# Kernel tuning notes

Measured on AMD Instinct MI355X. Metric: run time of the kernel, lower is better.

The kernel has to match this reference:

```python
import jax, jax.numpy as jnp
import numpy as np

B, H, W, D = 8, 32, 32, 512
NH = 8
DK = DV = 512
DKH = DK // NH
DVH = DV // NH


def setup_inputs() -> dict:
    key = jax.random.key(0)
    ks = jax.random.split(key, 16)
    s = 0.02
    return {
        "q": jax.random.normal(ks[0], (B, H, W, D), dtype=jnp.float32),
        "k": jax.random.normal(ks[1], (B, H, W, D), dtype=jnp.float32),
        "q_mask": jax.random.randint(ks[2], (B, H, W), 0, 2).astype(bool),
        "k_mask": jax.random.randint(ks[3], (B, H, W), 0, 2).astype(bool),
        "pos_logits": jax.random.normal(ks[4], (B, H, W, H, W), dtype=jnp.float32),
        "Wq": jax.random.normal(ks[5], (D, DK), dtype=jnp.float32) * s,
        "bq": jnp.zeros((DK,), dtype=jnp.float32),
        "Wk": jax.random.normal(ks[6], (D, DK), dtype=jnp.float32) * s,
        "bk": jnp.zeros((DK,), dtype=jnp.float32),
        "Wv": jax.random.normal(ks[7], (DK, DV), dtype=jnp.float32) * s,
        "bv": jnp.zeros((DV,), dtype=jnp.float32),
        "Wo": jax.random.normal(ks[8], (DV, D), dtype=jnp.float32) * s,
        "bo": jnp.zeros((D,), dtype=jnp.float32),
    }


def _split_heads(x, nh):
    b, h, w, d = x.shape
    return x.reshape(b, h, w, nh, d // nh).transpose(0, 3, 1, 2, 4)  # [B,Nh,H,W,dh]


def reference(q, k, q_mask, k_mask, pos_logits, Wq, bq, Wk, bk, Wv, bv, Wo, bo):
    b, h, w, d = q.shape
    qp = (q @ Wq + bq) * (DKH ** -0.5)
    kp = k @ Wk + bk
    vp = kp @ Wv + bv  # faithful quirk: v = projv(projk(k))
    qs = _split_heads(qp, NH)  # [B,Nh,H,W,dkh]
    ks_ = _split_heads(kp, NH)
    vs = _split_heads(vp, NH)  # [B,Nh,H,W,dvh]
    # additive mask: -inf where exactly one of q_mask[i,j], k_mask[k,l] is set
    xor = q_mask[:, :, :, None, None] ^ k_mask[:, None, None, :, :]  # [B,H,W,H,W]
    attn_mask = jnp.where(xor, -jnp.inf, 0.0)[:, None]  # [B,1,H,W,H,W]
    con = jnp.einsum('bhijd,bhkld->bhijkl', qs, ks_)  # [B,Nh,H,W,H,W]
    logits = attn_mask + con + pos_logits[:, None]
    weights = jax.nn.softmax(logits.reshape(b, NH, h, w, h * w), axis=-1)
    weights = weights.reshape(b, NH, h, w, h, w)
    attn = jnp.einsum('bhijkl,bhkld->bhijd', weights, vs)  # [B,Nh,H,W,dvh]
    attn = attn.transpose(0, 2, 3, 1, 4).reshape(b, h, w, NH * DVH)
    return attn @ Wo + bo  # dropout is identity at inference
```

## Files before the change

kernel.cpp:

```cpp
#include <hip/hip_runtime.h>
#include <hip/hip_bf16.h>
#include <math.h>

#define TOK 8192
#define DMODEL 512
#define SEQ 1024
#define NHEADS 8
#define DH 64
#define NBATCH 8

typedef __attribute__((ext_vector_type(8))) short short8v;
typedef __attribute__((ext_vector_type(4))) float f32x4;
typedef __attribute__((ext_vector_type(4))) int i32x4;

#define MFMA16(a, b, c) __builtin_amdgcn_mfma_f32_16x16x32_bf16(a, b, c, 0, 0, 0)

__device__ __forceinline__ unsigned short f2bf(float x) {
  __hip_bfloat16 h = __float2bfloat16(x);
  unsigned short u;
  __builtin_memcpy(&u, &h, 2);
  return u;
}
__device__ __forceinline__ unsigned int pk2(float a, float b) {
  return (unsigned int)f2bf(a) | ((unsigned int)f2bf(b) << 16);
}

__global__ __launch_bounds__(256) void wtr4_kernel(
    const float* __restrict__ W0, const float* __restrict__ W1,
    const float* __restrict__ W2, const float* __restrict__ W3,
    unsigned short* __restrict__ T0, unsigned short* __restrict__ T1,
    unsigned short* __restrict__ T2, unsigned short* __restrict__ T3) {
  __shared__ unsigned short tile[64][72];
  const int z = blockIdx.z;
  const float* W = (z == 0) ? W0 : (z == 1) ? W1 : (z == 2) ? W2 : W3;
  unsigned short* Wt = (z == 0) ? T0 : (z == 1) ? T1 : (z == 2) ? T2 : T3;
  const int kt = blockIdx.x, nt = blockIdx.y;
  const int t = threadIdx.x, r = t >> 2, c0 = (t & 3) * 16;
  const float* src = W + (size_t)(kt * 64 + r) * 512 + nt * 64 + c0;
  short8v v0, v1;
#pragma unroll
  for (int e = 0; e < 4; ++e) {
    float4 f = *reinterpret_cast<const float4*>(src + e * 4);
    short* dstv = (e < 2) ? (short*)&v0 : (short*)&v1;
    dstv[(e & 1) * 4 + 0] = (short)f2bf(f.x);
    dstv[(e & 1) * 4 + 1] = (short)f2bf(f.y);
    dstv[(e & 1) * 4 + 2] = (short)f2bf(f.z);
    dstv[(e & 1) * 4 + 3] = (short)f2bf(f.w);
  }
  *reinterpret_cast<short8v*>(&tile[r][c0]) = v0;
  *reinterpret_cast<short8v*>(&tile[r][c0 + 8]) = v1;
  __syncthreads();
  short8v o0, o1;
#pragma unroll
  for (int e = 0; e < 8; ++e) o0[e] = (short)tile[c0 + e][r];
#pragma unroll
  for (int e = 0; e < 8; ++e) o1[e] = (short)tile[c0 + 8 + e][r];
  unsigned short* dst = Wt + (size_t)(nt * 64 + r) * 512 + kt * 64 + c0;
  *reinterpret_cast<short8v*>(dst) = o0;
  *reinterpret_cast<short8v*>(dst + 8) = o1;
}

template <int AF32, int OUTMODE>
__device__ __forceinline__ void gemm_body(
    const void* __restrict__ Ap, const unsigned short* __restrict__ Wt,
    const float* __restrict__ bias, float scale, void* __restrict__ Cout) {
  __shared__ unsigned short Asl[128][72];
  __shared__ unsigned short Bsl[128][72];
  const int t = threadIdx.x;
  const int w = t >> 6, lane = t & 63, li = lane & 15, lg = lane >> 4;
  const int wr = w >> 1, wc = w & 1;
  const int rowBase = blockIdx.y * 128, colBase = blockIdx.x * 128;

  f32x4 zero4 = {0.f, 0.f, 0.f, 0.f};
  f32x4 acc[4][4];
#pragma unroll
  for (int mi = 0; mi < 4; ++mi)
#pragma unroll
    for (int nj = 0; nj < 4; ++nj) acc[mi][nj] = zero4;

  const int sr = t >> 1, sh = (t & 1) * 32;

  for (int k0 = 0; k0 < 512; k0 += 64) {
    if (AF32) {
      const float* src = reinterpret_cast<const float*>(Ap) +
                         (size_t)(rowBase + sr) * 512 + k0 + sh;
#pragma unroll
      for (int qq = 0; qq < 4; ++qq) {
        float4 f0 = *reinterpret_cast<const float4*>(src + qq * 8);
        float4 f1 = *reinterpret_cast<const float4*>(src + qq * 8 + 4);
        short8v o;
        o[0] = (short)f2bf(f0.x); o[1] = (short)f2bf(f0.y);
        o[2] = (short)f2bf(f0.z); o[3] = (short)f2bf(f0.w);
        o[4] = (short)f2bf(f1.x); o[5] = (short)f2bf(f1.y);
        o[6] = (short)f2bf(f1.z); o[7] = (short)f2bf(f1.w);
        *reinterpret_cast<short8v*>(&Asl[sr][sh + qq * 8]) = o;
      }
    } else {
      const unsigned short* src = reinterpret_cast<const unsigned short*>(Ap) +
                                  (size_t)(rowBase + sr) * 512 + k0 + sh;
#pragma unroll
      for (int qq = 0; qq < 4; ++qq)
        *reinterpret_cast<short8v*>(&Asl[sr][sh + qq * 8]) =
            *reinterpret_cast<const short8v*>(src + qq * 8);
    }
    {
      const unsigned short* src = Wt + (size_t)(colBase + sr) * 512 + k0 + sh;
#pragma unroll
      for (int qq = 0; qq < 4; ++qq)
        *reinterpret_cast<short8v*>(&Bsl[sr][sh + qq * 8]) =
            *reinterpret_cast<const short8v*>(src + qq * 8);
    }
    __syncthreads();
#pragma unroll
    for (int kk = 0; kk < 2; ++kk) {
      short8v af[4], bf[4];
#pragma unroll
      for (int mi = 0; mi < 4; ++mi)
        af[mi] = *reinterpret_cast<short8v*>(&Asl[wr * 64 + mi * 16 + li][kk * 32 + lg * 8]);
#pragma unroll
      for (int nj = 0; nj < 4; ++nj)
        bf[nj] = *reinterpret_cast<short8v*>(&Bsl[wc * 64 + nj * 16 + li][kk * 32 + lg * 8]);
#pragma unroll
      for (int mi = 0; mi < 4; ++mi)
#pragma unroll
        for (int nj = 0; nj < 4; ++nj) acc[mi][nj] = MFMA16(af[mi], bf[nj], acc[mi][nj]);
    }
    __syncthreads();
  }

#pragma unroll
  for (int nj = 0; nj < 4; ++nj) {
    const int col = colBase + wc * 64 + nj * 16 + li;
    const float bv = bias[col];
#pragma unroll
    for (int mi = 0; mi < 4; ++mi) {
      const int row0 = rowBase + wr * 64 + mi * 16 + lg * 4;
      if (OUTMODE == 2) {
        const int hh = col >> 6, dd = col & 63;
        const int bb = row0 >> 10, jj = row0 & 1023;
        unsigned short* dst =
            reinterpret_cast<unsigned short*>(Cout) +
            ((size_t)((bb * 8 + hh) * 64 + dd)) * SEQ + jj;
        float v0 = (acc[mi][nj][0] + bv) * scale;
        float v1 = (acc[mi][nj][1] + bv) * scale;
        float v2 = (acc[mi][nj][2] + bv) * scale;
        float v3 = (acc[mi][nj][3] + bv) * scale;
        *reinterpret_cast<uint2*>(dst) = make_uint2(pk2(v0, v1), pk2(v2, v3));
      } else {
#pragma unroll
        for (int rr = 0; rr < 4; ++rr) {
          const int row = row0 + rr;
          const float v = (acc[mi][nj][rr] + bv) * scale;
          if (OUTMODE == 1)
            reinterpret_cast<float*>(Cout)[(size_t)row * 512 + col] = v;
          else
            reinterpret_cast<unsigned short*>(Cout)[(size_t)row * 512 + col] = f2bf(v);
        }
      }
    }
  }
}

__global__ __launch_bounds__(256) void gemm_qk(
    const float* __restrict__ q, const float* __restrict__ k,
    const unsigned short* __restrict__ Wqt, const unsigned short* __restrict__ Wkt,
    const float* __restrict__ bq, const float* __restrict__ bk,
    unsigned short* __restrict__ qpb, unsigned short* __restrict__ kpb) {
  const int z = blockIdx.z;
  const void* A = z ? (const void*)k : (const void*)q;
  const unsigned short* Wt = z ? Wkt : Wqt;
  const float* bias = z ? bk : bq;
  const float scale = z ? 1.0f : 0.125f;
  void* C = z ? (void*)kpb : (void*)qpb;
  gemm_body<1, 0>(A, Wt, bias, scale, C);
}

__global__ __launch_bounds__(256) void gemm_vp(
    const unsigned short* __restrict__ kpb, const unsigned short* __restrict__ Wvt,
    const float* __restrict__ bv, unsigned short* __restrict__ vtb) {
  gemm_body<0, 2>(kpb, Wvt, bv, 1.0f, vtb);
}

__global__ __launch_bounds__(256) void gemm_out(
    const unsigned short* __restrict__ attnb, const unsigned short* __restrict__ Wot,
    const float* __restrict__ bo, float* __restrict__ out) {
  gemm_body<0, 1>(attnb, Wot, bo, 1.0f, out);
}

__global__ __launch_bounds__(512, 4) void attn_mfma(
    const unsigned short* __restrict__ qp, const unsigned short* __restrict__ kp,
    const unsigned short* __restrict__ vt, const float* __restrict__ pos,
    const int* __restrict__ qmask, const int* __restrict__ kmask,
    unsigned short* __restrict__ outb) {
  const int bx = blockIdx.x;
  const int qc = bx >> 6, h = (bx >> 3) & 7, b = bx & 7;
  const int t = threadIdx.x, w = t >> 6, lane = t & 63, li = lane & 15, lg = lane >> 4;
  const int qrow = qc * 128 + w * 16;

  __shared__ unsigned short Kl[64 * 72];
  __shared__ unsigned short Vl[64 * 72];
  __shared__ unsigned short Pl[8][16 * 72];

  const size_t qg = (size_t)(b * SEQ + qrow + li) * DMODEL + h * DH;
  const short8v qf0 = *reinterpret_cast<const short8v*>(qp + qg + lg * 8);
  const short8v qf1 = *reinterpret_cast<const short8v*>(qp + qg + 32 + lg * 8);
  const int qmv = qmask[b * SEQ + qrow + li];

  f32x4 zero4 = {0.f, 0.f, 0.f, 0.f};
  f32x4 acc_o[4];
#pragma unroll
  for (int n = 0; n < 4; ++n) acc_o[n] = zero4;
  float m = -3e38f, l = 0.f;

  const int srow = t >> 3, schk = (t & 7) * 8;
  const unsigned short* kgp = kp + (size_t)(b * SEQ + srow) * DMODEL + h * DH + schk;
  const unsigned short* vgp = vt + ((size_t)((b * 8 + h) * 64) + srow) * SEQ + schk;
  const int sldst = srow * 72 + schk;

  const float* posb = pos + (size_t)(b * SEQ + qrow + li) * SEQ;
  const int* kmb = kmask + b * SEQ;

  {
    short8v kr = *reinterpret_cast<const short8v*>(kgp);
    short8v vr = *reinterpret_cast<const short8v*>(vgp);
    *reinterpret_cast<short8v*>(&Kl[sldst]) = kr;
    *reinterpret_cast<short8v*>(&Vl[sldst]) = vr;
  }
  __syncthreads();

  for (int kt = 0; kt < 16; ++kt) {
    const int kbase = kt * 64;

    short8v kr, vr;
    if (kt < 15) {
      kr = *reinterpret_cast<const short8v*>(kgp + (size_t)(kbase + 64) * DMODEL);
      vr = *reinterpret_cast<const short8v*>(vgp + kbase + 64);
    }

    f32x4 pvn[4];
    i32x4 kmn[4];
#pragma unroll
    for (int n = 0; n < 4; ++n) {
      pvn[n] = *reinterpret_cast<const f32x4*>(posb + kbase + n * 16 + lg * 4);
      kmn[n] = *reinterpret_cast<const i32x4*>(kmb + kbase + n * 16 + lg * 4);
    }

    f32x4 x4[4];
    __builtin_amdgcn_s_setprio(1);
#pragma unroll
    for (int n = 0; n < 4; ++n) {
      short8v kfa = *reinterpret_cast<short8v*>(&Kl[(n * 16 + li) * 72 + lg * 8]);
      short8v kfb = *reinterpret_cast<short8v*>(&Kl[(n * 16 + li) * 72 + 32 + lg * 8]);
      x4[n] = MFMA16(kfa, qf0, zero4);
      x4[n] = MFMA16(kfb, qf1, x4[n]);
    }
    __builtin_amdgcn_s_setprio(0);

    float x[4][4];
    float tm = -3e38f;
#pragma unroll
    for (int n = 0; n < 4; ++n)
#pragma unroll
      for (int r = 0; r < 4; ++r) {
        float xx = x4[n][r] + pvn[n][r];
        if ((qmv != 0) != (kmn[n][r] != 0)) xx = -1e30f;
        x[n][r] = xx;
        tm = fmaxf(tm, xx);
      }
    tm = fmaxf(tm, __shfl_xor(tm, 16));
    tm = fmaxf(tm, __shfl_xor(tm, 32));
    const float mn = fmaxf(m, tm);
    const float rs = __expf(m - mn);
    m = mn;
    float psum = 0.f;
#pragma unroll
    for (int n = 0; n < 4; ++n)
#pragma unroll
      for (int r = 0; r < 4; ++r) {
        const float p = __expf(x[n][r] - m);
        x[n][r] = p;
        psum += p;
      }
    psum += __shfl_xor(psum, 16);
    psum += __shfl_xor(psum, 32);
    l = l * rs + psum;
    float rsb[4];
#pragma unroll
    for (int r = 0; r < 4; ++r) rsb[r] = __shfl(rs, lg * 4 + r, 16);
#pragma unroll
    for (int n = 0; n < 4; ++n)
#pragma unroll
      for (int r = 0; r < 4; ++r) acc_o[n][r] *= rsb[r];

#pragma unroll
    for (int n = 0; n < 4; ++n) {
      *reinterpret_cast<uint2*>(&Pl[w][li * 72 + n * 16 + lg * 4]) =
          make_uint2(pk2(x[n][0], x[n][1]), pk2(x[n][2], x[n][3]));
    }
    asm volatile("s_waitcnt lgkmcnt(0)" ::: "memory");
    __builtin_amdgcn_sched_barrier(0);
    const short8v pf0 = *reinterpret_cast<short8v*>(&Pl[w][li * 72 + lg * 8]);
    const short8v pf1 = *reinterpret_cast<short8v*>(&Pl[w][li * 72 + 32 + lg * 8]);

    __builtin_amdgcn_s_setprio(1);
#pragma unroll
    for (int n = 0; n < 4; ++n) {
      short8v vfa = *reinterpret_cast<short8v*>(&Vl[(n * 16 + li) * 72 + lg * 8]);
      short8v vfb = *reinterpret_cast<short8v*>(&Vl[(n * 16 + li) * 72 + 32 + lg * 8]);
      acc_o[n] = MFMA16(pf0, vfa, acc_o[n]);
      acc_o[n] = MFMA16(pf1, vfb, acc_o[n]);
    }
    __builtin_amdgcn_s_setprio(0);

    if (kt < 15) {
      __syncthreads();
      *reinterpret_cast<short8v*>(&Kl[sldst]) = kr;
      *reinterpret_cast<short8v*>(&Vl[sldst]) = vr;
      __syncthreads();
    }
  }

  const float linv = 1.f / l;
  float lb[4];
#pragma unroll
  for (int r = 0; r < 4; ++r) lb[r] = __shfl(linv, lg * 4 + r, 16);
  unsigned short* ob = outb + (size_t)(b * SEQ + qrow) * DMODEL + h * DH;
#pragma unroll
  for (int n = 0; n < 4; ++n)
#pragma unroll
    for (int r = 0; r < 4; ++r)
      ob[(size_t)(lg * 4 + r) * DMODEL + n * 16 + li] = f2bf(acc_o[n][r] * lb[r]);
}

extern "C" void kernel_launch(void* const* d_in, const int* in_sizes, int n_in,
                              void* d_out, int out_size, void* d_ws, size_t ws_size,
                              hipStream_t stream) {
  const float* q   = (const float*)d_in[0];
  const float* k   = (const float*)d_in[1];
  const int*   qm  = (const int*)d_in[2];
  const int*   km  = (const int*)d_in[3];
  const float* pos = (const float*)d_in[4];
  const float* Wq  = (const float*)d_in[5];
  const float* bq  = (const float*)d_in[6];
  const float* Wk  = (const float*)d_in[7];
  const float* bk  = (const float*)d_in[8];
  const float* Wv  = (const float*)d_in[9];
  const float* bv  = (const float*)d_in[10];
  const float* Wo  = (const float*)d_in[11];
  const float* bo  = (const float*)d_in[12];
  float* out = (float*)d_out;

  char* ws = (char*)d_ws;
  const size_t MB8 = (size_t)TOK * DMODEL * 2;
  unsigned short* qpb   = (unsigned short*)(ws);
  unsigned short* kpb   = (unsigned short*)(ws + 1 * MB8);
  unsigned short* attnb = (unsigned short*)(ws + 2 * MB8);
  unsigned short* vtb   = (unsigned short*)(ws + 3 * MB8);
  unsigned short* Wqt   = (unsigned short*)(ws + 4 * MB8);
  unsigned short* Wkt   = Wqt + (size_t)512 * 512;
  unsigned short* Wvt   = Wkt + (size_t)512 * 512;
  unsigned short* Wot   = Wvt + (size_t)512 * 512;

  hipLaunchKernelGGL(wtr4_kernel, dim3(8, 8, 4), dim3(256), 0, stream,
                     Wq, Wk, Wv, Wo, Wqt, Wkt, Wvt, Wot);

  const dim3 ggrid(DMODEL / 128, TOK / 128);
  hipLaunchKernelGGL(gemm_qk, dim3(4, 64, 2), dim3(256), 0, stream,
                     q, k, Wqt, Wkt, bq, bk, qpb, kpb);
  hipLaunchKernelGGL(gemm_vp, ggrid, dim3(256), 0, stream, kpb, Wvt, bv, vtb);

  hipLaunchKernelGGL(attn_mfma, dim3(512), dim3(512), 0, stream,
                     qpb, kpb, vtb, pos, qm, km, attnb);

  hipLaunchKernelGGL(gemm_out, ggrid, dim3(256), 0, stream, attnb, Wot, bo, out);
}
```

Measured before the change: 127.8 us.

## Give each attention wave two 16-row query groups and use smaller 128-thread blocks

The attention kernel now has each wave process 32 query rows as two 16-row groups. Each K and V fragment read from LDS is reused across two MFMAs, halving LDS fragment reads per MFMA and adding independent MFMA chains. Blocks shrink from 8 waves to 2 waves covering 64 rows, with twice as many blocks. In exchange, each K/V tile is staged from global memory twice as often overall, register pressure rises, and there are fewer waves per block to hide latency.

```diff
diff --git a/kernel.cpp b/kernel.cpp
--- a/kernel.cpp
+++ b/kernel.cpp
@@ -187,7 +187,7 @@
   gemm_body<0, 1>(attnb, Wot, bo, 1.0f, out);
 }
 
-__global__ __launch_bounds__(512, 4) void attn_mfma(
+__global__ __launch_bounds__(128, 2) void attn_mfma(
     const unsigned short* __restrict__ qp, const unsigned short* __restrict__ kp,
     const unsigned short* __restrict__ vt, const float* __restrict__ pos,
     const int* __restrict__ qmask, const int* __restrict__ kmask,
@@ -195,141 +195,174 @@
   const int bx = blockIdx.x;
   const int qc = bx >> 6, h = (bx >> 3) & 7, b = bx & 7;
   const int t = threadIdx.x, w = t >> 6, lane = t & 63, li = lane & 15, lg = lane >> 4;
-  const int qrow = qc * 128 + w * 16;
+  const int qrow = qc * 64 + w * 32;
 
   __shared__ unsigned short Kl[64 * 72];
   __shared__ unsigned short Vl[64 * 72];
-  __shared__ unsigned short Pl[8][16 * 72];
-
-  const size_t qg = (size_t)(b * SEQ + qrow + li) * DMODEL + h * DH;
-  const short8v qf0 = *reinterpret_cast<const short8v*>(qp + qg + lg * 8);
-  const short8v qf1 = *reinterpret_cast<const short8v*>(qp + qg + 32 + lg * 8);
-  const int qmv = qmask[b * SEQ + qrow + li];
+  __shared__ unsigned short Pl[4][16 * 72];
+
+  short8v qf[2][2];
+  int qmv[2];
+#pragma unroll
+  for (int g = 0; g < 2; ++g) {
+    const size_t qg = (size_t)(b * SEQ + qrow + g * 16 + li) * DMODEL + h * DH;
+    qf[g][0] = *reinterpret_cast<const short8v*>(qp + qg + lg * 8);
+    qf[g][1] = *reinterpret_cast<const short8v*>(qp + qg + 32 + lg * 8);
+    qmv[g] = qmask[b * SEQ + qrow + g * 16 + li];
+  }
 
   f32x4 zero4 = {0.f, 0.f, 0.f, 0.f};
-  f32x4 acc_o[4];
-#pragma unroll
-  for (int n = 0; n < 4; ++n) acc_o[n] = zero4;
-  float m = -3e38f, l = 0.f;
-
-  const int srow = t >> 3, schk = (t & 7) * 8;
+  f32x4 acc_o[2][4];
+#pragma unroll
+  for (int g = 0; g < 2; ++g)
+#pragma unroll
+    for (int n = 0; n < 4; ++n) acc_o[g][n] = zero4;
+  float m[2] = {-3e38f, -3e38f}, l[2] = {0.f, 0.f};
+
+  const int srow = t >> 1, schk = (t & 1) * 32;
   const unsigned short* kgp = kp + (size_t)(b * SEQ + srow) * DMODEL + h * DH + schk;
   const unsigned short* vgp = vt + ((size_t)((b * 8 + h) * 64) + srow) * SEQ + schk;
   const int sldst = srow * 72 + schk;
 
-  const float* posb = pos + (size_t)(b * SEQ + qrow + li) * SEQ;
+  const float* posb0 = pos + (size_t)(b * SEQ + qrow + li) * SEQ;
+  const float* posb1 = posb0 + (size_t)16 * SEQ;
   const int* kmb = kmask + b * SEQ;
 
   {
-    short8v kr = *reinterpret_cast<const short8v*>(kgp);
-    short8v vr = *reinterpret_cast<const short8v*>(vgp);
-    *reinterpret_cast<short8v*>(&Kl[sldst]) = kr;
-    *reinterpret_cast<short8v*>(&Vl[sldst]) = vr;
+#pragma unroll
+    for (int qq = 0; qq < 4; ++qq) {
+      *reinterpret_cast<short8v*>(&Kl[sldst + qq * 8]) =
+          *reinterpret_cast<const short8v*>(kgp + qq * 8);
+      *reinterpret_cast<short8v*>(&Vl[sldst + qq * 8]) =
+          *reinterpret_cast<const short8v*>(vgp + qq * 8);
+    }
   }
   __syncthreads();
 
   for (int kt = 0; kt < 16; ++kt) {
     const int kbase = kt * 64;
 
-    short8v kr, vr;
+    short8v kr[4], vr[4];
     if (kt < 15) {
-      kr = *reinterpret_cast<const short8v*>(kgp + (size_t)(kbase + 64) * DMODEL);
-      vr = *reinterpret_cast<const short8v*>(vgp + kbase + 64);
-    }
-
-    f32x4 pvn[4];
+#pragma unroll
+      for (int qq = 0; qq < 4; ++qq) {
+        kr[qq] = *reinterpret_cast<const short8v*>(kgp + (size_t)(kbase + 64) * DMODEL + qq * 8);
+        vr[qq] = *reinterpret_cast<const short8v*>(vgp + kbase + 64 + qq * 8);
+      }
+    }
+
+    f32x4 pvn[2][4];
     i32x4 kmn[4];
 #pragma unroll
     for (int n = 0; n < 4; ++n) {
-      pvn[n] = *reinterpret_cast<const f32x4*>(posb + kbase + n * 16 + lg * 4);
+      pvn[0][n] = *reinterpret_cast<const f32x4*>(posb0 + kbase + n * 16 + lg * 4);
+      pvn[1][n] = *reinterpret_cast<const f32x4*>(posb1 + kbase + n * 16 + lg * 4);
       kmn[n] = *reinterpret_cast<const i32x4*>(kmb + kbase + n * 16 + lg * 4);
     }
 
-    f32x4 x4[4];
+    f32x4 x4[2][4];
     __builtin_amdgcn_s_setprio(1);
 #pragma unroll
     for (int n = 0; n < 4; ++n) {
       short8v kfa = *reinterpret_cast<short8v*>(&Kl[(n * 16 + li) * 72 + lg * 8]);
       short8v kfb = *reinterpret_cast<short8v*>(&Kl[(n * 16 + li) * 72 + 32 + lg * 8]);
-      x4[n] = MFMA16(kfa, qf0, zero4);
-      x4[n] = MFMA16(kfb, qf1, x4[n]);
+      x4[0][n] = MFMA16(kfa, qf[0][0], zero4);
+      x4[1][n] = MFMA16(kfa, qf[1][0], zero4);
+      x4[0][n] = MFMA16(kfb, qf[0][1], x4[0][n]);
+      x4[1][n] = MFMA16(kfb, qf[1][1], x4[1][n]);
     }
     __builtin_amdgcn_s_setprio(0);
 
-    float x[4][4];
-    float tm = -3e38f;
-#pragma unroll
-    for (int n = 0; n < 4; ++n)
-#pragma unroll
-      for (int r = 0; r < 4; ++r) {
-        float xx = x4[n][r] + pvn[n][r];
-        if ((qmv != 0) != (kmn[n][r] != 0)) xx = -1e30f;
-        x[n][r] = xx;
-        tm = fmaxf(tm, xx);
+#pragma unroll
+    for (int g = 0; g < 2; ++g) {
+      float x[4][4];
+      float tm = -3e38f;
+#pragma unroll
+      for (int n = 0; n < 4; ++n)
+#pragma unroll
+        for (int r = 0; r < 4; ++r) {
+          float xx = x4[g][n][r] + pvn[g][n][r];
+          if ((qmv[g] != 0) != (kmn[n][r] != 0)) xx = -1e30f;
+          x[n][r] = xx;
+          tm = fmaxf(tm, xx);
+        }
+      tm = fmaxf(tm, __shfl_xor(tm, 16));
+      tm = fmaxf(tm, __shfl_xor(tm, 32));
+      const float mn = fmaxf(m[g], tm);
+      const float rs = __expf(m[g] - mn);
+      m[g] = mn;
+      float psum = 0.f;
+#pragma unroll
+      for (int n = 0; n < 4; ++n)
+#pragma unroll
+        for (int r = 0; r < 4; ++r) {
+          const float p = __expf(x[n][r] - m[g]);
+          x[n][r] = p;
+          psum += p;
+        }
+      psum += __shfl_xor(psum, 16);
+      psum += __shfl_xor(psum, 32);
+      l[g] = l[g] * rs + psum;
+      float rsb[4];
+#pragma unroll
+      for (int r = 0; r < 4; ++r) rsb[r] = __shfl(rs, lg * 4 + r, 16);
+#pragma unroll
+      for (int n = 0; n < 4; ++n)
+#pragma unroll
+        for (int r = 0; r < 4; ++r) acc_o[g][n][r] *= rsb[r];
+
+#pragma unroll
+      for (int n = 0; n < 4; ++n) {
+        *reinterpret_cast<uint2*>(&Pl[w * 2 + g][li * 72 + n * 16 + lg * 4]) =
+            make_uint2(pk2(x[n][0], x[n][1]), pk2(x[n][2], x[n][3]));
       }
-    tm = fmaxf(tm, __shfl_xor(tm, 16));
-    tm = fmaxf(tm, __shfl_xor(tm, 32));
-    const float mn = fmaxf(m, tm);
-    const float rs = __expf(m - mn);
-    m = mn;
-    float psum = 0.f;
-#pragma unroll
-    for (int n = 0; n < 4; ++n)
-#pragma unroll
-      for (int r = 0; r < 4; ++r) {
-        const float p = __expf(x[n][r] - m);
-        x[n][r] = p;
-        psum += p;
-      }
-    psum += __shfl_xor(psum, 16);
-    psum += __shfl_xor(psum, 32);
-    l = l * rs + psum;
-    float rsb[4];
-#pragma unroll
-    for (int r = 0; r < 4; ++r) rsb[r] = __shfl(rs, lg * 4 + r, 16);
-#pragma unroll
-    for (int n = 0; n < 4; ++n)
-#pragma unroll
-      for (int r = 0; r < 4; ++r) acc_o[n][r] *= rsb[r];
-
-#pragma unroll
-    for (int n = 0; n < 4; ++n) {
-      *reinterpret_cast<uint2*>(&Pl[w][li * 72 + n * 16 + lg * 4]) =
-          make_uint2(pk2(x[n][0], x[n][1]), pk2(x[n][2], x[n][3]));
     }
     asm volatile("s_waitcnt lgkmcnt(0)" ::: "memory");
     __builtin_amdgcn_sched_barrier(0);
-    const short8v pf0 = *reinterpret_cast<short8v*>(&Pl[w][li * 72 + lg * 8]);
-    const short8v pf1 = *reinterpret_cast<short8v*>(&Pl[w][li * 72 + 32 + lg * 8]);
+
+    short8v pf[2][2];
+#pragma unroll
+    for (int g = 0; g < 2; ++g) {
+      pf[g][0] = *reinterpret_cast<short8v*>(&Pl[w * 2 + g][li * 72 + lg * 8]);
+      pf[g][1] = *reinterpret_cast<short8v*>(&Pl[w * 2 + g][li * 72 + 32 + lg * 8]);
+    }
 
     __builtin_amdgcn_s_setprio(1);
 #pragma unroll
     for (int n = 0; n < 4; ++n) {
       short8v vfa = *reinterpret_cast<short8v*>(&Vl[(n * 16 + li) * 72 + lg * 8]);
       short8v vfb = *reinterpret_cast<short8v*>(&Vl[(n * 16 + li) * 72 + 32 + lg * 8]);
-      acc_o[n] = MFMA16(pf0, vfa, acc_o[n]);
-      acc_o[n] = MFMA16(pf1, vfb, acc_o[n]);
+      acc_o[0][n] = MFMA16(pf[0][0], vfa, acc_o[0][n]);
+      acc_o[1][n] = MFMA16(pf[1][0], vfa, acc_o[1][n]);
+      acc_o[0][n] = MFMA16(pf[0][1], vfb, acc_o[0][n]);
+      acc_o[1][n] = MFMA16(pf[1][1], vfb, acc_o[1][n]);
     }
     __builtin_amdgcn_s_setprio(0);
 
     if (kt < 15) {
       __syncthreads();
-      *reinterpret_cast<short8v*>(&Kl[sldst]) = kr;
-      *reinterpret_cast<short8v*>(&Vl[sldst]) = vr;
+#pragma unroll
+      for (int qq = 0; qq < 4; ++qq) {
+        *reinterpret_cast<short8v*>(&Kl[sldst + qq * 8]) = kr[qq];
+        *reinterpret_cast<short8v*>(&Vl[sldst + qq * 8]) = vr[qq];
+      }
       __syncthreads();
     }
   }
 
-  const float linv = 1.f / l;
-  float lb[4];
-#pragma unroll
-  for (int r = 0; r < 4; ++r) lb[r] = __shfl(linv, lg * 4 + r, 16);
-  unsigned short* ob = outb + (size_t)(b * SEQ + qrow) * DMODEL + h * DH;
-#pragma unroll
-  for (int n = 0; n < 4; ++n)
-#pragma unroll
-    for (int r = 0; r < 4; ++r)
-      ob[(size_t)(lg * 4 + r) * DMODEL + n * 16 + li] = f2bf(acc_o[n][r] * lb[r]);
+#pragma unroll
+  for (int g = 0; g < 2; ++g) {
+    const float linv = 1.f / l[g];
+    float lb[4];
+#pragma unroll
+    for (int r = 0; r < 4; ++r) lb[r] = __shfl(linv, lg * 4 + r, 16);
+    unsigned short* ob = outb + (size_t)(b * SEQ + qrow + g * 16) * DMODEL + h * DH;
+#pragma unroll
+    for (int n = 0; n < 4; ++n)
+#pragma unroll
+      for (int r = 0; r < 4; ++r)
+        ob[(size_t)(lg * 4 + r) * DMODEL + n * 16 + li] = f2bf(acc_o[g][n][r] * lb[r]);
+  }
 }
 
 extern "C" void kernel_launch(void* const* d_in, const int* in_sizes, int n_in,
@@ -369,7 +402,7 @@
                      q, k, Wqt, Wkt, bq, bk, qpb, kpb);
   hipLaunchKernelGGL(gemm_vp, ggrid, dim3(256), 0, stream, kpb, Wvt, bv, vtb);
 
-  hipLaunchKernelGGL(attn_mfma, dim3(512), dim3(512), 0, stream,
+  hipLaunchKernelGGL(attn_mfma, dim3(1024), dim3(128), 0, stream,
                      qpb, kpb, vtb, pos, qm, km, attnb);
 
   hipLaunchKernelGGL(gemm_out, ggrid, dim3(256), 0, stream, attnb, Wot, bo, out);
```

Measured after the change: 135.1 us. 1.06x slower.

## Prefetch next K-tile into registers during MFMA in projection GEMM

Applied to the files above, without the earlier changes.

Restructures the projection GEMM main loop to issue global loads for the next 64-wide K tile into registers before the MFMA compute on the current tile, then store them to shared memory after a barrier. This overlaps global memory latency with matrix-core work instead of serializing load-sync-compute. It raises register pressure (up to 8 float4 plus 8 short8v per thread), which may reduce occupancy.

```diff
diff --git a/kernel.cpp b/kernel.cpp
--- a/kernel.cpp
+++ b/kernel.cpp
@@ -79,15 +79,19 @@
     for (int nj = 0; nj < 4; ++nj) acc[mi][nj] = zero4;
 
   const int sr = t >> 1, sh = (t & 1) * 32;
-
-  for (int k0 = 0; k0 < 512; k0 += 64) {
+  const float* af32base =
+      AF32 ? reinterpret_cast<const float*>(Ap) + (size_t)(rowBase + sr) * 512 + sh : nullptr;
+  const unsigned short* abf16base =
+      AF32 ? nullptr
+           : reinterpret_cast<const unsigned short*>(Ap) + (size_t)(rowBase + sr) * 512 + sh;
+  const unsigned short* bbase = Wt + (size_t)(colBase + sr) * 512 + sh;
+
+  {
     if (AF32) {
-      const float* src = reinterpret_cast<const float*>(Ap) +
-                         (size_t)(rowBase + sr) * 512 + k0 + sh;
 #pragma unroll
       for (int qq = 0; qq < 4; ++qq) {
-        float4 f0 = *reinterpret_cast<const float4*>(src + qq * 8);
-        float4 f1 = *reinterpret_cast<const float4*>(src + qq * 8 + 4);
+        float4 f0 = *reinterpret_cast<const float4*>(af32base + qq * 8);
+        float4 f1 = *reinterpret_cast<const float4*>(af32base + qq * 8 + 4);
         short8v o;
         o[0] = (short)f2bf(f0.x); o[1] = (short)f2bf(f0.y);
         o[2] = (short)f2bf(f0.z); o[3] = (short)f2bf(f0.w);
@@ -96,21 +100,41 @@
         *reinterpret_cast<short8v*>(&Asl[sr][sh + qq * 8]) = o;
       }
     } else {
-      const unsigned short* src = reinterpret_cast<const unsigned short*>(Ap) +
-                                  (size_t)(rowBase + sr) * 512 + k0 + sh;
 #pragma unroll
       for (int qq = 0; qq < 4; ++qq)
         *reinterpret_cast<short8v*>(&Asl[sr][sh + qq * 8]) =
-            *reinterpret_cast<const short8v*>(src + qq * 8);
-    }
-    {
-      const unsigned short* src = Wt + (size_t)(colBase + sr) * 512 + k0 + sh;
+            *reinterpret_cast<const short8v*>(abf16base + qq * 8);
+    }
+#pragma unroll
+    for (int qq = 0; qq < 4; ++qq)
+      *reinterpret_cast<short8v*>(&Bsl[sr][sh + qq * 8]) =
+          *reinterpret_cast<const short8v*>(bbase + qq * 8);
+  }
+  __syncthreads();
+
+  for (int kt = 0; kt < 8; ++kt) {
+    const int knext = (kt + 1) * 64;
+
+    float4 paf[8];
+    short8v pab[4];
+    short8v pbb[4];
+    if (kt < 7) {
+      if (AF32) {
+#pragma unroll
+        for (int qq = 0; qq < 4; ++qq) {
+          paf[2 * qq]     = *reinterpret_cast<const float4*>(af32base + knext + qq * 8);
+          paf[2 * qq + 1] = *reinterpret_cast<const float4*>(af32base + knext + qq * 8 + 4);
+        }
+      } else {
+#pragma unroll
+        for (int qq = 0; qq < 4; ++qq)
+          pab[qq] = *reinterpret_cast<const short8v*>(abf16base + knext + qq * 8);
+      }
 #pragma unroll
       for (int qq = 0; qq < 4; ++qq)
-        *reinterpret_cast<short8v*>(&Bsl[sr][sh + qq * 8]) =
-            *reinterpret_cast<const short8v*>(src + qq * 8);
-    }
-    __syncthreads();
+        pbb[qq] = *reinterpret_cast<const short8v*>(bbase + knext + qq * 8);
+    }
+
 #pragma unroll
     for (int kk = 0; kk < 2; ++kk) {
       short8v af[4], bf[4];
@@ -125,7 +149,30 @@
 #pragma unroll
         for (int nj = 0; nj < 4; ++nj) acc[mi][nj] = MFMA16(af[mi], bf[nj], acc[mi][nj]);
     }
-    __syncthreads();
+
+    if (kt < 7) {
+      __syncthreads();
+      if (AF32) {
+#pragma unroll
+        for (int qq = 0; qq < 4; ++qq) {
+          const float4 f0 = paf[2 * qq], f1 = paf[2 * qq + 1];
+          short8v o;
+          o[0] = (short)f2bf(f0.x); o[1] = (short)f2bf(f0.y);
+          o[2] = (short)f2bf(f0.z); o[3] = (short)f2bf(f0.w);
+          o[4] = (short)f2bf(f1.x); o[5] = (short)f2bf(f1.y);
+          o[6] = (short)f2bf(f1.z); o[7] = (short)f2bf(f1.w);
+          *reinterpret_cast<short8v*>(&Asl[sr][sh + qq * 8]) = o;
+        }
+      } else {
+#pragma unroll
+        for (int qq = 0; qq < 4; ++qq)
+          *reinterpret_cast<short8v*>(&Asl[sr][sh + qq * 8]) = pab[qq];
+      }
+#pragma unroll
+      for (int qq = 0; qq < 4; ++qq)
+        *reinterpret_cast<short8v*>(&Bsl[sr][sh + qq * 8]) = pbb[qq];
+      __syncthreads();
+    }
   }
 
 #pragma unroll
```

Result: faster. 110.6 us (-13.5%).
